# Kernel optimization log

Measured on AMD Instinct MI355X. Metric: run time of the kernel, lower is better.

Reference implementation:

```python
import jax, jax.numpy as jnp
import numpy as np
import math

D_MODEL = 512
MAX_PIXELS = 900
MAX_GRIDS_IN_PAIR = 2
MAX_PAIRS = 16
B, S = 8, 16384
N_GRIDS, GRID_LEN = 32, 512   # 32 * 512 = 16384 = S
N_PAIRS, PAIR_LEN = 16, 1024  # 16 * 1024 = 16384 = S


def _sinusoid_pe(length, d_model):
    # matches torch: pe[:,0::2]=sin(pos*div), pe[:,1::2]=cos(pos*div)
    pos = np.arange(length, dtype=np.float32)[:, None]
    div = np.exp(np.arange(0, d_model, 2, dtype=np.float32) * (-math.log(10000.0) / d_model))
    pe = np.zeros((length, d_model), dtype=np.float32)
    pe[:, 0::2] = np.sin(pos * div)
    pe[:, 1::2] = np.cos(pos * div)
    return jnp.asarray(pe)


def setup_inputs() -> dict:
    key = jax.random.key(0)
    x = jax.random.normal(key, (B, S, D_MODEL), dtype=jnp.float32)
    grid_starts = jnp.arange(N_GRIDS, dtype=jnp.int32) * GRID_LEN
    grid_lengths = jnp.full((N_GRIDS,), GRID_LEN, dtype=jnp.int32)
    pair_starts = jnp.arange(N_PAIRS, dtype=jnp.int32) * PAIR_LEN
    pair_lengths = jnp.full((N_PAIRS,), PAIR_LEN, dtype=jnp.int32)
    return {
        "x": x,
        "pixels_pe": _sinusoid_pe(MAX_PIXELS, D_MODEL),   # [max_pixels, D]
        "grids_pe": _sinusoid_pe(MAX_GRIDS_IN_PAIR, D_MODEL),  # [2, D]
        "pairs_pe": _sinusoid_pe(MAX_PAIRS, D_MODEL),     # [max_pairs, D]
        "grid_starts": grid_starts,
        "grid_lengths": grid_lengths,
        "pair_starts": pair_starts,
        "pair_lengths": pair_lengths,
    }


def reference(x, pixels_pe, grids_pe, pairs_pe, grid_starts, grid_lengths, pair_starts, pair_lengths):
    S_ = x.shape[1]
    pos = jnp.arange(S_, dtype=jnp.int32)

    # map each position to its grid segment (starts are sorted, starts[0]==0)
    gid = jnp.searchsorted(grid_starts, pos, side="right") - 1          # [S]
    goff = pos - grid_starts[gid]                                        # within-grid pixel index
    gmask = (goff < grid_lengths[gid])[:, None]                          # covered by a grid segment

    pix = jnp.where(gmask, pixels_pe[jnp.clip(goff, 0, pixels_pe.shape[0] - 1)], 0.0)  # [S,D]
    grd = jnp.where(gmask, grids_pe[gid % 2], 0.0)                       # [S,D]

    # map each position to its pair segment
    pid = jnp.searchsorted(pair_starts, pos, side="right") - 1
    poff = pos - pair_starts[pid]
    pmask = (poff < pair_lengths[pid])[:, None]
    pr = jnp.where(pmask, pairs_pe[jnp.clip(pid, 0, pairs_pe.shape[0] - 1)], 0.0)      # [S,D]

    combined = pix + grd + pr                                            # [S,D]
    return x + combined[None, :, :]                                      # broadcast over batch
```

## Files before the change

### kernel.cpp

```cpp
#include <hip/hip_runtime.h>
#include <hip/hip_bf16.h>
#include <stdint.h>

#define D_MODEL    512
#define S_LEN      16384
#define B_SZ       8
#define N_GRIDS    32
#define N_PAIRS    16
#define MAX_PIXELS 900

#define CHUNKS_PER_ROW (D_MODEL / 8)
#define TOTAL_CHUNKS   (S_LEN * CHUNKS_PER_ROW)

__device__ __forceinline__ float bf16u_to_f32(uint32_t lo16) {
    union { uint32_t u; float f; } c;
    c.u = lo16 << 16;
    return c.f;
}

__device__ __forceinline__ uint16_t f32_to_bf16_rne(float f) {
    union { float f; uint32_t u; } c; c.f = f;
    uint32_t u = c.u;
    u += 0x7FFFu + ((u >> 16) & 1u);
    return (uint16_t)(u >> 16);
}

__device__ __forceinline__ uint32_t pack2_bf16(float lo, float hi) {
    return (uint32_t)f32_to_bf16_rne(lo) | ((uint32_t)f32_to_bf16_rne(hi) << 16);
}

__global__ __launch_bounds__(256) void PositionalEncoding_30915174597069_kernel(
    const void* __restrict__ x,
    const void* __restrict__ pixels_pe,
    const void* __restrict__ grids_pe,
    const void* __restrict__ pairs_pe,
    const int* __restrict__ grid_starts,
    const int* __restrict__ grid_lengths,
    const int* __restrict__ pair_starts,
    const int* __restrict__ pair_lengths,
    void* __restrict__ out)
{
    const int chunk = blockIdx.x * blockDim.x + threadIdx.x;
    if (chunk >= TOTAL_CHUNKS) return;

    const int s = chunk >> 6;
    const int d = (chunk & 63) << 3;

    int gid = 0;
    #pragma unroll
    for (int sh = 4; sh >= 0; --sh) {
        int cand = gid + (1 << sh);
        if (cand < N_GRIDS && grid_starts[cand] <= s) gid = cand;
    }
    const int goff   = s - grid_starts[gid];
    const bool gmask = goff < grid_lengths[gid];
    const int pixrow = min(goff, MAX_PIXELS - 1);

    int pid = 0;
    #pragma unroll
    for (int sh = 3; sh >= 0; --sh) {
        int cand = pid + (1 << sh);
        if (cand < N_PAIRS && pair_starts[cand] <= s) pid = cand;
    }
    const int poff   = s - pair_starts[pid];
    const bool pmask = poff < pair_lengths[pid];

    union { uint32_t u; float f; } probe;
    probe.u = ((const uint32_t*)pixels_pe)[D_MODEL];
    const bool is_f32 = (probe.f > 0.82f && probe.f < 0.86f);

    const size_t bstride = (size_t)S_LEN * D_MODEL;
    const size_t base    = (size_t)s * D_MODEL + d;

    if (is_f32) {
        const float* pxp = (const float*)pixels_pe + (size_t)pixrow   * D_MODEL + d;
        const float* gdp = (const float*)grids_pe  + (size_t)(gid & 1) * D_MODEL + d;
        const float* prp = (const float*)pairs_pe  + (size_t)pid      * D_MODEL + d;

        float comb[8];
        {
            float4 pxv0 = ((const float4*)pxp)[0], pxv1 = ((const float4*)pxp)[1];
            float4 gdv0 = ((const float4*)gdp)[0], gdv1 = ((const float4*)gdp)[1];
            float4 prv0 = ((const float4*)prp)[0], prv1 = ((const float4*)prp)[1];
            const float* px = (const float*)&pxv0;
            const float* px1 = (const float*)&pxv1;
            const float* gd0 = (const float*)&gdv0, *gd1 = (const float*)&gdv1;
            const float* pr0 = (const float*)&prv0, *pr1 = (const float*)&prv1;
            #pragma unroll
            for (int j = 0; j < 4; ++j) {
                float a0 = gmask ? px[j]  : 0.0f;
                float g0 = gmask ? gd0[j] : 0.0f;
                float p0 = pmask ? pr0[j] : 0.0f;
                comb[j] = (a0 + g0) + p0;
                float a1 = gmask ? px1[j] : 0.0f;
                float g1 = gmask ? gd1[j] : 0.0f;
                float p1 = pmask ? pr1[j] : 0.0f;
                comb[4 + j] = (a1 + g1) + p1;
            }
        }

        const float* xf = (const float*)x;
        float*       of = (float*)out;

        float4 xv[2 * B_SZ];
        #pragma unroll
        for (int b = 0; b < B_SZ; ++b) {
            const float4* p = (const float4*)(xf + base + (size_t)b * bstride);
            xv[2*b]     = p[0];
            xv[2*b + 1] = p[1];
        }
        #pragma unroll
        for (int b = 0; b < B_SZ; ++b) {
            float4 o0, o1;
            const float* xi0 = (const float*)&xv[2*b];
            const float* xi1 = (const float*)&xv[2*b + 1];
            float* o0f = (float*)&o0; float* o1f = (float*)&o1;
            #pragma unroll
            for (int j = 0; j < 4; ++j) {
                o0f[j] = xi0[j] + comb[j];
                o1f[j] = xi1[j] + comb[4 + j];
            }
            float4* op = (float4*)(of + base + (size_t)b * bstride);
            op[0] = o0;
            op[1] = o1;
        }
    } else {
        const uint16_t* xh  = (const uint16_t*)x;
        uint16_t*       oh  = (uint16_t*)out;
        const uint4 pxv = *(const uint4*)((const uint16_t*)pixels_pe + (size_t)pixrow    * D_MODEL + d);
        const uint4 gdv = *(const uint4*)((const uint16_t*)grids_pe  + (size_t)(gid & 1) * D_MODEL + d);
        const uint4 prv = *(const uint4*)((const uint16_t*)pairs_pe  + (size_t)pid       * D_MODEL + d);
        const float gm = gmask ? 1.0f : 0.0f;
        const float pm = pmask ? 1.0f : 0.0f;

        float comb[8];
        {
            const uint32_t* px = (const uint32_t*)&pxv;
            const uint32_t* gd = (const uint32_t*)&gdv;
            const uint32_t* pr = (const uint32_t*)&prv;
            #pragma unroll
            for (int j = 0; j < 4; ++j) {
                float px_lo = bf16u_to_f32(px[j] & 0xFFFFu), px_hi = bf16u_to_f32(px[j] >> 16);
                float gd_lo = bf16u_to_f32(gd[j] & 0xFFFFu), gd_hi = bf16u_to_f32(gd[j] >> 16);
                float pr_lo = bf16u_to_f32(pr[j] & 0xFFFFu), pr_hi = bf16u_to_f32(pr[j] >> 16);
                comb[2*j]     = gm * (px_lo + gd_lo) + pm * pr_lo;
                comb[2*j + 1] = gm * (px_hi + gd_hi) + pm * pr_hi;
            }
        }

        uint4 xv[B_SZ];
        #pragma unroll
        for (int b = 0; b < B_SZ; ++b)
            xv[b] = *(const uint4*)(xh + base + (size_t)b * bstride);

        #pragma unroll
        for (int b = 0; b < B_SZ; ++b) {
            const uint32_t* xi = (const uint32_t*)&xv[b];
            uint4 ov;
            uint32_t* oi = (uint32_t*)&ov;
            #pragma unroll
            for (int j = 0; j < 4; ++j) {
                float lo = bf16u_to_f32(xi[j] & 0xFFFFu) + comb[2*j];
                float hi = bf16u_to_f32(xi[j] >> 16)     + comb[2*j + 1];
                oi[j] = pack2_bf16(lo, hi);
            }
            *(uint4*)(oh + base + (size_t)b * bstride) = ov;
        }
    }
}

extern "C" void kernel_launch(void* const* d_in, const int* in_sizes, int n_in,
                              void* d_out, int out_size, void* d_ws, size_t ws_size,
                              hipStream_t stream) {
    const void* x         = d_in[0];
    const void* pixels_pe = d_in[1];
    const void* grids_pe  = d_in[2];
    const void* pairs_pe  = d_in[3];
    const int* grid_starts  = (const int*)d_in[4];
    const int* grid_lengths = (const int*)d_in[5];
    const int* pair_starts  = (const int*)d_in[6];
    const int* pair_lengths = (const int*)d_in[7];

    const int threads = 256;
    const int blocks  = (TOTAL_CHUNKS + threads - 1) / threads;
    hipLaunchKernelGGL(PositionalEncoding_30915174597069_kernel,
                       dim3(blocks), dim3(threads), 0, stream,
                       x, pixels_pe, grids_pe, pairs_pe,
                       grid_starts, grid_lengths, pair_starts, pair_lengths,
                       d_out);
}
```

Measured before the change: 449.4 us.

## Spread batch dimension across grid y and scalarize per-row segment lookup

The per-thread loop over the 8 batch entries is removed. The batch index now comes from blockIdx.y, so each thread handles one batch row chunk and the launch has 8x as many blocks. The row index is made wave-uniform with readfirstlane, so the grid and pair searches can run on the scalar unit. The aim is more parallelism and fewer live registers per thread, at the cost of re-reading the positional-encoding rows once per batch entry, which should mostly hit in cache.

```diff
diff --git a/kernel.cpp b/kernel.cpp
--- a/kernel.cpp
+++ b/kernel.cpp
@@ -41,10 +41,12 @@
     void* __restrict__ out)
 {
     const int chunk = blockIdx.x * blockDim.x + threadIdx.x;
-    if (chunk >= TOTAL_CHUNKS) return;
+    const int b     = blockIdx.y;
 
-    const int s = chunk >> 6;
-    const int d = (chunk & 63) << 3;
+    const int s_v = chunk >> 6;
+    const int d   = (chunk & 63) << 3;
+
+    const int s = __builtin_amdgcn_readfirstlane(s_v);
 
     int gid = 0;
     #pragma unroll
@@ -71,101 +73,65 @@
 
     const size_t bstride = (size_t)S_LEN * D_MODEL;
     const size_t base    = (size_t)s * D_MODEL + d;
+    const size_t off     = base + (size_t)b * bstride;
 
     if (is_f32) {
-        const float* pxp = (const float*)pixels_pe + (size_t)pixrow   * D_MODEL + d;
+        const float* pxp = (const float*)pixels_pe + (size_t)pixrow    * D_MODEL + d;
         const float* gdp = (const float*)grids_pe  + (size_t)(gid & 1) * D_MODEL + d;
-        const float* prp = (const float*)pairs_pe  + (size_t)pid      * D_MODEL + d;
+        const float* prp = (const float*)pairs_pe  + (size_t)pid       * D_MODEL + d;
+        const float* xf  = (const float*)x + off;
+        float*       of  = (float*)out + off;
 
-        float comb[8];
-        {
-            float4 pxv0 = ((const float4*)pxp)[0], pxv1 = ((const float4*)pxp)[1];
-            float4 gdv0 = ((const float4*)gdp)[0], gdv1 = ((const float4*)gdp)[1];
-            float4 prv0 = ((const float4*)prp)[0], prv1 = ((const float4*)prp)[1];
-            const float* px = (const float*)&pxv0;
-            const float* px1 = (const float*)&pxv1;
-            const float* gd0 = (const float*)&gdv0, *gd1 = (const float*)&gdv1;
-            const float* pr0 = (const float*)&prv0, *pr1 = (const float*)&prv1;
-            #pragma unroll
-            for (int j = 0; j < 4; ++j) {
-                float a0 = gmask ? px[j]  : 0.0f;
-                float g0 = gmask ? gd0[j] : 0.0f;
-                float p0 = pmask ? pr0[j] : 0.0f;
-                comb[j] = (a0 + g0) + p0;
-                float a1 = gmask ? px1[j] : 0.0f;
-                float g1 = gmask ? gd1[j] : 0.0f;
-                float p1 = pmask ? pr1[j] : 0.0f;
-                comb[4 + j] = (a1 + g1) + p1;
-            }
+        float4 xv0 = ((const float4*)xf)[0];
+        float4 xv1 = ((const float4*)xf)[1];
+        float4 pxv0 = ((const float4*)pxp)[0], pxv1 = ((const float4*)pxp)[1];
+        float4 gdv0 = ((const float4*)gdp)[0], gdv1 = ((const float4*)gdp)[1];
+        float4 prv0 = ((const float4*)prp)[0], prv1 = ((const float4*)prp)[1];
+
+        const float* x0 = (const float*)&xv0, *x1 = (const float*)&xv1;
+        const float* px0 = (const float*)&pxv0, *px1 = (const float*)&pxv1;
+        const float* gd0 = (const float*)&gdv0, *gd1 = (const float*)&gdv1;
+        const float* pr0 = (const float*)&prv0, *pr1 = (const float*)&prv1;
+
+        float4 o0, o1;
+        float* o0f = (float*)&o0; float* o1f = (float*)&o1;
+        #pragma unroll
+        for (int j = 0; j < 4; ++j) {
+            float c0 = ((gmask ? px0[j] : 0.0f) + (gmask ? gd0[j] : 0.0f)) + (pmask ? pr0[j] : 0.0f);
+            float c1 = ((gmask ? px1[j] : 0.0f) + (gmask ? gd1[j] : 0.0f)) + (pmask ? pr1[j] : 0.0f);
+            o0f[j] = x0[j] + c0;
+            o1f[j] = x1[j] + c1;
         }
+        ((float4*)of)[0] = o0;
+        ((float4*)of)[1] = o1;
+    } else {
+        const uint16_t* xh = (const uint16_t*)x + off;
+        uint16_t*       oh = (uint16_t*)out + off;
 
-        const float* xf = (const float*)x;
-        float*       of = (float*)out;
-
-        float4 xv[2 * B_SZ];
-        #pragma unroll
-        for (int b = 0; b < B_SZ; ++b) {
-            const float4* p = (const float4*)(xf + base + (size_t)b * bstride);
-            xv[2*b]     = p[0];
-            xv[2*b + 1] = p[1];
-        }
-        #pragma unroll
-        for (int b = 0; b < B_SZ; ++b) {
-            float4 o0, o1;
-            const float* xi0 = (const float*)&xv[2*b];
-            const float* xi1 = (const float*)&xv[2*b + 1];
-            float* o0f = (float*)&o0; float* o1f = (float*)&o1;
-            #pragma unroll
-            for (int j = 0; j < 4; ++j) {
-                o0f[j] = xi0[j] + comb[j];
-                o1f[j] = xi1[j] + comb[4 + j];
-            }
-            float4* op = (float4*)(of + base + (size_t)b * bstride);
-            op[0] = o0;
-            op[1] = o1;
-        }
-    } else {
-        const uint16_t* xh  = (const uint16_t*)x;
-        uint16_t*       oh  = (uint16_t*)out;
+        const uint4 xv  = *(const uint4*)xh;
         const uint4 pxv = *(const uint4*)((const uint16_t*)pixels_pe + (size_t)pixrow    * D_MODEL + d);
         const uint4 gdv = *(const uint4*)((const uint16_t*)grids_pe  + (size_t)(gid & 1) * D_MODEL + d);
         const uint4 prv = *(const uint4*)((const uint16_t*)pairs_pe  + (size_t)pid       * D_MODEL + d);
         const float gm = gmask ? 1.0f : 0.0f;
         const float pm = pmask ? 1.0f : 0.0f;
 
-        float comb[8];
-        {
-            const uint32_t* px = (const uint32_t*)&pxv;
-            const uint32_t* gd = (const uint32_t*)&gdv;
-            const uint32_t* pr = (const uint32_t*)&prv;
-            #pragma unroll
-            for (int j = 0; j < 4; ++j) {
-                float px_lo = bf16u_to_f32(px[j] & 0xFFFFu), px_hi = bf16u_to_f32(px[j] >> 16);
-                float gd_lo = bf16u_to_f32(gd[j] & 0xFFFFu), gd_hi = bf16u_to_f32(gd[j] >> 16);
-                float pr_lo = bf16u_to_f32(pr[j] & 0xFFFFu), pr_hi = bf16u_to_f32(pr[j] >> 16);
-                comb[2*j]     = gm * (px_lo + gd_lo) + pm * pr_lo;
-                comb[2*j + 1] = gm * (px_hi + gd_hi) + pm * pr_hi;
-            }
+        const uint32_t* xi = (const uint32_t*)&xv;
+        const uint32_t* px = (const uint32_t*)&pxv;
+        const uint32_t* gd = (const uint32_t*)&gdv;
+        const uint32_t* pr = (const uint32_t*)&prv;
+        uint4 ov;
+        uint32_t* oi = (uint32_t*)&ov;
+        #pragma unroll
+        for (int j = 0; j < 4; ++j) {
+            float c_lo = gm * (bf16u_to_f32(px[j] & 0xFFFFu) + bf16u_to_f32(gd[j] & 0xFFFFu))
+                       + pm * bf16u_to_f32(pr[j] & 0xFFFFu);
+            float c_hi = gm * (bf16u_to_f32(px[j] >> 16) + bf16u_to_f32(gd[j] >> 16))
+                       + pm * bf16u_to_f32(pr[j] >> 16);
+            float lo = bf16u_to_f32(xi[j] & 0xFFFFu) + c_lo;
+            float hi = bf16u_to_f32(xi[j] >> 16)     + c_hi;
+            oi[j] = pack2_bf16(lo, hi);
         }
-
-        uint4 xv[B_SZ];
-        #pragma unroll
-        for (int b = 0; b < B_SZ; ++b)
-            xv[b] = *(const uint4*)(xh + base + (size_t)b * bstride);
-
-        #pragma unroll
-        for (int b = 0; b < B_SZ; ++b) {
-            const uint32_t* xi = (const uint32_t*)&xv[b];
-            uint4 ov;
-            uint32_t* oi = (uint32_t*)&ov;
-            #pragma unroll
-            for (int j = 0; j < 4; ++j) {
-                float lo = bf16u_to_f32(xi[j] & 0xFFFFu) + comb[2*j];
-                float hi = bf16u_to_f32(xi[j] >> 16)     + comb[2*j + 1];
-                oi[j] = pack2_bf16(lo, hi);
-            }
-            *(uint4*)(oh + base + (size_t)b * bstride) = ov;
-        }
+        *(uint4*)oh = ov;
     }
 }
 
@@ -182,9 +148,9 @@
     const int* pair_lengths = (const int*)d_in[7];
 
     const int threads = 256;
-    const int blocks  = (TOTAL_CHUNKS + threads - 1) / threads;
+    const int blocks_x = TOTAL_CHUNKS / threads;
     hipLaunchKernelGGL(PositionalEncoding_30915174597069_kernel,
-                       dim3(blocks), dim3(threads), 0, stream,
+                       dim3(blocks_x, B_SZ), dim3(threads), 0, stream,
                        x, pixels_pe, grids_pe, pairs_pe,
                        grid_starts, grid_lengths, pair_starts, pair_lengths,
                        d_out);
```

After: 453.2 us. Within noise of the previous version (+0.9%).
